# Performance work log

Hardware: AMD Instinct MI355X
Metric: run time of the kernel (lower is better)

Reference implementation:

```python
import jax, jax.numpy as jnp
import numpy as np

EPS = 1e-12  # torch F.normalize eps


def setup_inputs() -> dict:
    key = jax.random.key(0)
    k1, k2, k3, k4, k5 = jax.random.split(key, 5)
    N, C, H, W = 32, 512, 32, 32
    E = 1024   # expansion * dim
    G = 8      # group
    D = E // G # 128, per-group channel dim
    K = 64     # num_clusters
    x = jax.random.normal(k1, (N, C, H, W), dtype=jnp.float32)
    W1 = jax.random.normal(k2, (E, C), dtype=jnp.float32) / np.sqrt(C)
    W2 = jax.random.normal(k3, (G, E), dtype=jnp.float32) / np.sqrt(E)
    Wc = jax.random.normal(k4, (K, D), dtype=jnp.float32) / np.sqrt(D)
    centroids = jax.random.uniform(k5, (K, D), dtype=jnp.float32)
    return {"x": x, "W1": W1, "W2": W2, "Wc": Wc, "centroids": centroids}


def reference(x, W1, W2, Wc, centroids):
    # x: [N, C, H, W]; W1: [E, C]; W2: [G, E]; Wc: [K, D]; centroids: [K, D]
    N, C, H, W = x.shape
    E = W1.shape[0]
    G = W2.shape[0]
    K, D = Wc.shape
    P = H * W
    # descriptor-wise L2 normalization over channel dim
    norm = jnp.linalg.norm(x, axis=1, keepdims=True)
    x = x / jnp.maximum(norm, EPS)
    # linear1 on channels: [N, E, P]
    xe = jnp.einsum('ncp,ec->nep', x.reshape(N, C, P), W1)
    # grouped features: [N, G, D, P]
    xg = xe.reshape(N, G, D, P)
    # attention gate: sigmoid(linear2)  -> [N, G, P]
    att = jax.nn.sigmoid(jnp.einsum('nep,ge->ngp', xe, W2))
    # 1x1 conv = per-pixel matmul with cluster weights -> [N, G, K, P]
    soft_assign = jax.nn.softmax(jnp.einsum('ngdp,kd->ngkp', xg, Wc), axis=2)
    # combined per-(cluster,pixel) weight
    w = soft_assign * att[:, :, None, :]  # [N, G, K, P]
    # NetVLAD residual aggregation, algebraically decomposed to avoid the
    # giant [N,G,K,D,P] intermediate:
    #   vlad[n,k,d] = sum_{g,p} w * xg  -  centroids[k,d] * sum_{g,p} w
    agg = jnp.einsum('ngkp,ngdp->nkd', w, xg)  # [N, K, D]
    wsum = w.sum(axis=(1, 3))                  # [N, K]
    vlad = agg - wsum[:, :, None] * centroids[None]  # [N, K, D]
    return vlad.reshape(N, K * D)
```

## Files before the change

### kernel.cpp

```cpp
#include <hip/hip_runtime.h>


#define N_  32
#define C_  512
#define P_  1024
#define E_  1024
#define G_  8
#define D_  128
#define K_  64

typedef __attribute__((ext_vector_type(8))) short bf16x8;
typedef __attribute__((ext_vector_type(4))) float f32x4;

__device__ __forceinline__ unsigned short f2b(float f) {
    union { float f; unsigned u; } v; v.f = f;
    unsigned r = (v.u + 0x7FFFu + ((v.u >> 16) & 1u)) >> 16;
    return (unsigned short)r;
}
__device__ __forceinline__ float b2f(unsigned short h) {
    union { unsigned u; float f; } v; v.u = ((unsigned)h) << 16;
    return v.f;
}

__device__ __forceinline__ void gl_lds16(const void* g, void* l) {
    __builtin_amdgcn_global_load_lds(
        (const __attribute__((address_space(1))) void*)g,
        (__attribute__((address_space(3))) void*)l, 16, 0, 0);
}

#define SB  __builtin_amdgcn_sched_barrier(0)
#define BAR __builtin_amdgcn_s_barrier()
#define WAITV(n_) asm volatile("s_waitcnt vmcnt(" #n_ ")" ::: "memory")

__global__ __launch_bounds__(256) void k0_prep(const float* __restrict__ W1,
                                               const float* __restrict__ Wc,
                                               const float* __restrict__ W2,
                                               unsigned short* __restrict__ W1b,
                                               unsigned short* __restrict__ Vb,
                                               unsigned short* __restrict__ Wa) {
    int bid = blockIdx.x;
    int t = threadIdx.x;
    if (bid < 1024) {
        int i0 = bid * 512 + t;
        W1b[i0]       = f2b(W1[i0]);
        W1b[i0 + 256] = f2b(W1[i0 + 256]);
        int ch = bid & 1, k = (bid >> 1) & 63, g = bid >> 7;
        int c = ch * 256 + t;
        float acc = 0.f;
        #pragma unroll 8
        for (int d = 0; d < 128; ++d)
            acc += Wc[k * 128 + d] * W1[(g * 128 + d) * C_ + c];
        Vb[(g * 64 + k) * C_ + c] = f2b(acc);
    } else {
        __shared__ float red[256];
        int idx = bid - 1024;
        int g  = idx >> 4;
        int c0 = (idx & 15) * 32;
        int c  = c0 + (t & 31);
        int ec = t >> 5;
        float acc = 0.f;
        #pragma unroll 8
        for (int i = 0; i < 128; ++i) {
            int e = ec * 128 + i;
            acc += W2[g * E_ + e] * W1[e * C_ + c];
        }
        red[t] = acc;
        __syncthreads();
        if (t < 32) {
            float s = 0.f;
            #pragma unroll
            for (int j = 0; j < 8; ++j) s += red[j * 32 + t];
            Wa[g * C_ + c0 + t] = f2b(s);
        }
    }
}

__global__ __launch_bounds__(256) void k1_norm_transpose(const float* __restrict__ x,
                                                         unsigned short* __restrict__ xhat_t) {
    __shared__ short xc[128 * 256];
    __shared__ float red[256];
    __shared__ float rn[64];
    int n = blockIdx.y;
    int p0 = blockIdx.x * 64;
    int t = threadIdx.x;
    int ps = t & 63, cs = t >> 6;

    float ss = 0.f;
    for (int i = 0; i < 128; ++i) {
        float v = x[((size_t)(n * C_ + cs * 128 + i)) * P_ + p0 + ps];
        ss += v * v;
        xc[i * 256 + t] = (short)f2b(v);
    }
    red[t] = ss;
    __syncthreads();
    if (t < 64) {
        float s = red[t] + red[64 + t] + red[128 + t] + red[192 + t];
        rn[t] = 1.0f / fmaxf(sqrtf(s), 1e-12f);
    }
    __syncthreads();

    float r = rn[ps];
    size_t base = ((size_t)(n * P_ + p0 + ps)) * C_ + cs * 128;
    #pragma unroll
    for (int jj = 0; jj < 16; ++jj) {
        bf16x8 o;
        #pragma unroll
        for (int j = 0; j < 8; ++j)
            o[j] = (short)f2b(b2f((unsigned short)xc[(jj * 8 + j) * 256 + t]) * r);
        *(bf16x8*)&xhat_t[base + jj * 8] = o;
    }
}

__global__ __launch_bounds__(256) void k2_gemm_xe(const unsigned short* __restrict__ W1b,
                                                  const unsigned short* __restrict__ xhat_t,
                                                  unsigned short* __restrict__ xe) {
    __shared__ __align__(16) short As[128 * 64];
    __shared__ __align__(16) short Bs[128 * 64];
    int n = blockIdx.y;
    int e0 = (blockIdx.x >> 3) * 128;
    int p0 = (blockIdx.x & 7) * 128;
    int t = threadIdx.x;
    int w = t >> 6, l = t & 63, q = l >> 4, l15 = l & 15;
    int wr = w >> 1, wc = w & 1;

    f32x4 acc[4][4];
    #pragma unroll
    for (int mi = 0; mi < 4; ++mi)
        #pragma unroll
        for (int ni = 0; ni < 4; ++ni)
            acc[mi][ni] = (f32x4){0.f, 0.f, 0.f, 0.f};

    for (int ks = 0; ks < 8; ++ks) {
        int k0 = ks * 64;
        #pragma unroll
        for (int i = 0; i < 4; ++i) {
            int ch = i * 256 + t;
            int row = ch >> 3, c8 = ch & 7;
            gl_lds16(&W1b[(e0 + row) * C_ + k0 + ((c8 ^ (row & 7)) * 8)], &As[ch * 8]);
        }
        #pragma unroll
        for (int i = 0; i < 4; ++i) {
            int ch = i * 256 + t;
            int row = ch >> 3, c8 = ch & 7;
            gl_lds16(&xhat_t[((size_t)(n * P_ + p0 + row)) * C_ + k0 + ((c8 ^ (row & 7)) * 8)], &Bs[ch * 8]);
        }
        __syncthreads();

        #pragma unroll
        for (int kk = 0; kk < 2; ++kk) {
            bf16x8 af[4], bf[4];
            #pragma unroll
            for (int mi = 0; mi < 4; ++mi)
                af[mi] = *(const bf16x8*)&As[(wr * 64 + mi * 16 + l15) * 64 + (((kk * 4 + q) ^ (l15 & 7)) * 8)];
            #pragma unroll
            for (int ni = 0; ni < 4; ++ni)
                bf[ni] = *(const bf16x8*)&Bs[(wc * 64 + ni * 16 + l15) * 64 + (((kk * 4 + q) ^ (l15 & 7)) * 8)];
            #pragma unroll
            for (int mi = 0; mi < 4; ++mi)
                #pragma unroll
                for (int ni = 0; ni < 4; ++ni)
                    acc[mi][ni] = __builtin_amdgcn_mfma_f32_16x16x32_bf16(af[mi], bf[ni], acc[mi][ni], 0, 0, 0);
        }
        __syncthreads();
    }

    #pragma unroll
    for (int mi = 0; mi < 4; ++mi) {
        #pragma unroll
        for (int ni = 0; ni < 4; ++ni) {
            #pragma unroll
            for (int r = 0; r < 4; ++r) {
                int e = e0 + wr * 64 + mi * 16 + q * 4 + r;
                int p = p0 + wc * 64 + ni * 16 + l15;
                xe[((size_t)(n * E_ + e)) * P_ + p] = f2b(acc[mi][ni][r]);
            }
        }
    }
}

__global__ __launch_bounds__(256) void k3n_att(const unsigned short* __restrict__ Wa,
                                               const unsigned short* __restrict__ xhat_t,
                                               float* __restrict__ att_s) {
    __shared__ __align__(16) short xh[64 * 512];
    __shared__ __align__(16) short wal[8 * 520];
    int n = blockIdx.y;
    int p0 = blockIdx.x * 64;
    int t = threadIdx.x;
    int w = t >> 6, l = t & 63, q = l >> 4, l15 = l & 15;

    #pragma unroll
    for (int i = 0; i < 16; ++i) {
        int ch = i * 256 + t;
        int row = ch >> 6, s = ch & 63;
        gl_lds16(&xhat_t[((size_t)(n * P_ + p0 + row)) * C_ + ((s ^ (row & 7)) * 8)],
                 &xh[ch * 8]);
    }
    #pragma unroll
    for (int i = 0; i < 2; ++i) {
        int ch = i * 256 + t;
        int row = ch >> 6, c8 = ch & 63;
        gl_lds16(&Wa[row * C_ + c8 * 8], &wal[row * 520 + c8 * 8]);
    }
    __syncthreads();

    f32x4 acc = (f32x4){0.f, 0.f, 0.f, 0.f};
    const bf16x8 zf = {};
    #pragma unroll
    for (int kstep = 0; kstep < 16; ++kstep) {
        bf16x8 av = *(const bf16x8*)&wal[(l15 & 7) * 520 + (kstep * 4 + q) * 8];
        bf16x8 af = (l15 < 8) ? av : zf;
        int row = w * 16 + l15;
        bf16x8 bf = *(const bf16x8*)&xh[row * 512 + (((kstep * 4 + q) ^ (row & 7)) * 8)];
        acc = __builtin_amdgcn_mfma_f32_16x16x32_bf16(af, bf, acc, 0, 0, 0);
    }

    if (q < 2) {
        int p = p0 + w * 16 + l15;
        #pragma unroll
        for (int r = 0; r < 4; ++r) {
            int g = q * 4 + r;
            att_s[((size_t)(n * G_ + g)) * P_ + p] = 1.0f / (1.0f + __expf(-acc[r]));
        }
    }
}

__device__ __forceinline__ void stage_s(short* sb, const unsigned short* __restrict__ Vb,
                                        const unsigned short* __restrict__ xhat_t,
                                        int g, int n, int p0c, int k0, int t) {
    {
        int row = t >> 3, c8 = t & 7;
        gl_lds16(&Vb[(g * 64 + row) * C_ + k0 + ((c8 ^ (row & 7)) * 8)], &sb[t * 8]);
    }
    #pragma unroll
    for (int i = 0; i < 2; ++i) {
        int ch = i * 512 + t;
        int row = ch >> 3, c8 = ch & 7;
        gl_lds16(&xhat_t[((size_t)(n * P_ + p0c + row)) * C_ + k0 + ((c8 ^ (row & 7)) * 8)],
                 &sb[4096 + ch * 8]);
    }
}

__device__ __forceinline__ void stage_xg(short* xglds, const unsigned short* __restrict__ xe,
                                         int n, int g, int p0c, int t) {
    #pragma unroll
    for (int i = 0; i < 4; ++i) {
        int ch = i * 512 + t;
        int row = ch >> 4, c16 = ch & 15;
        gl_lds16(&xe[((size_t)(n * E_ + g * 128 + row)) * P_ + p0c + ((c16 ^ (row & 7)) * 8)],
                 &xglds[ch * 8]);
    }
}

__device__ __forceinline__ void mfma_s(f32x4 acc[4], const short* sb, int w, int q, int l15) {
    #pragma unroll
    for (int kk = 0; kk < 2; ++kk) {
        bf16x8 af[4], bfr;
        #pragma unroll
        for (int mi = 0; mi < 4; ++mi)
            af[mi] = *(const bf16x8*)&sb[(mi * 16 + l15) * 64 + (((kk * 4 + q) ^ (l15 & 7)) * 8)];
        bfr = *(const bf16x8*)&sb[4096 + (w * 16 + l15) * 64 + (((kk * 4 + q) ^ (l15 & 7)) * 8)];
        #pragma unroll
        for (int mi = 0; mi < 4; ++mi)
            acc[mi] = __builtin_amdgcn_mfma_f32_16x16x32_bf16(af[mi], bfr, acc[mi], 0, 0, 0);
    }
}

__global__ __launch_bounds__(512, 4) void k4_assign_agg(const unsigned short* __restrict__ Vb,
                                                        const unsigned short* __restrict__ xhat_t,
                                                        const unsigned short* __restrict__ xe,
                                                        const float* __restrict__ att_s,
                                                        float* __restrict__ agg_part,
                                                        float* __restrict__ wsum_part) {
    __shared__ __align__(16) char smem[81920];
    short* S0    = (short*)smem;
    short* S1    = (short*)(smem + 24576);
    short* xglds = (short*)(smem + 49152);
    short* wlds  = (short*)smem;
    float* wred  = (float*)smem;

    int b = blockIdx.y * 16 + blockIdx.x;
    int work = (b & 7) * 64 + (b >> 3);
    int n = work >> 4, g = work & 7, ph = (work >> 3) & 1;

    int t = threadIdx.x;
    int w = t >> 6, l = t & 63, q = l >> 4, l15 = l & 15;
    int kh = w >> 2, dq = w & 3;

    f32x4 acc_a[2][2];
    #pragma unroll
    for (int mi = 0; mi < 2; ++mi)
        #pragma unroll
        for (int ni = 0; ni < 2; ++ni)
            acc_a[mi][ni] = (f32x4){0.f, 0.f, 0.f, 0.f};
    float wsp[16];
    #pragma unroll
    for (int j = 0; j < 16; ++j) wsp[j] = 0.f;

#define RND(CUR, NXT, KN) \
    stage_s(NXT, Vb, xhat_t, g, n, p0c, (KN) * 64, t); \
    WAITV(3); BAR; SB; \
    mfma_s(acc_s, CUR, w, q, l15); \
    BAR; SB;

    #pragma unroll 1
    for (int cc = 0; cc < 4; ++cc) {
        int p0c = ph * 512 + cc * 128;

        float av = att_s[(((size_t)(n * G_ + g)) * P_) + p0c + w * 16 + l15];

        f32x4 acc_s[4];
        #pragma unroll
        for (int mi = 0; mi < 4; ++mi)
            acc_s[mi] = (f32x4){0.f, 0.f, 0.f, 0.f};

        stage_s(S0, Vb, xhat_t, g, n, p0c, 0, t);
        RND(S0, S1, 1)
        RND(S1, S0, 2)
        RND(S0, S1, 3)
        RND(S1, S0, 4)
        RND(S0, S1, 5)
        RND(S1, S0, 6)
        stage_s(S1, Vb, xhat_t, g, n, p0c, 448, t);
        stage_xg(xglds, xe, n, g, p0c, t);
        WAITV(7); BAR; SB;
        mfma_s(acc_s, S0, w, q, l15);
        BAR; SB;
        WAITV(4); BAR; SB;
        mfma_s(acc_s, S1, w, q, l15);
        BAR; SB;

        {
            float m = -1e30f;
            #pragma unroll
            for (int mi = 0; mi < 4; ++mi)
                #pragma unroll
                for (int r = 0; r < 4; ++r)
                    m = fmaxf(m, acc_s[mi][r]);
            m = fmaxf(m, __shfl_xor(m, 16));
            m = fmaxf(m, __shfl_xor(m, 32));
            float s = 0.f;
            #pragma unroll
            for (int mi = 0; mi < 4; ++mi)
                #pragma unroll
                for (int r = 0; r < 4; ++r) {
                    float e = __expf(acc_s[mi][r] - m);
                    acc_s[mi][r] = e;
                    s += e;
                }
            s += __shfl_xor(s, 16);
            s += __shfl_xor(s, 32);

            float scale = av / s;

            #pragma unroll
            for (int mi = 0; mi < 4; ++mi)
                #pragma unroll
                for (int r = 0; r < 4; ++r) {
                    float wv = acc_s[mi][r] * scale;
                    wsp[mi * 4 + r] += wv;
                    wlds[(mi * 16 + q * 4 + r) * 136 + (w * 16 + l15)] = (short)f2b(wv);
                }
        }
        __syncthreads();

        #pragma unroll
        for (int pk = 0; pk < 4; ++pk) {
            bf16x8 a2[2], b2[2];
            #pragma unroll
            for (int mi = 0; mi < 2; ++mi)
                a2[mi] = *(const bf16x8*)&wlds[(kh * 32 + mi * 16 + l15) * 136 + pk * 32 + q * 8];
            #pragma unroll
            for (int ni = 0; ni < 2; ++ni)
                b2[ni] = *(const bf16x8*)&xglds[(dq * 32 + ni * 16 + l15) * 128
                                                + (((pk * 4 + q) ^ (l15 & 7)) * 8)];
            #pragma unroll
            for (int mi = 0; mi < 2; ++mi)
                #pragma unroll
                for (int ni = 0; ni < 2; ++ni)
                    acc_a[mi][ni] = __builtin_amdgcn_mfma_f32_16x16x32_bf16(a2[mi], b2[ni], acc_a[mi][ni], 0, 0, 0);
        }
        __syncthreads();
    }

    size_t base = (((size_t)(n * G_ + g)) * 2 + ph) * 64;
    #pragma unroll
    for (int mi = 0; mi < 2; ++mi)
        #pragma unroll
        for (int ni = 0; ni < 2; ++ni)
            #pragma unroll
            for (int r = 0; r < 4; ++r) {
                int k = kh * 32 + mi * 16 + q * 4 + r;
                int d = dq * 32 + ni * 16 + l15;
                agg_part[(base + k) * 128 + d] = acc_a[mi][ni][r];
            }

    #pragma unroll
    for (int j = 0; j < 16; ++j) {
        float v = wsp[j];
        v += __shfl_xor(v, 1);
        v += __shfl_xor(v, 2);
        v += __shfl_xor(v, 4);
        v += __shfl_xor(v, 8);
        if (l15 == 0) {
            int k = (j >> 2) * 16 + q * 4 + (j & 3);
            wred[w * 64 + k] = v;
        }
    }
    __syncthreads();
    if (t < 64) {
        float s = 0.f;
        #pragma unroll
        for (int wv = 0; wv < 8; ++wv)
            s += wred[wv * 64 + t];
        wsum_part[(((size_t)(n * G_ + g)) * 2 + ph) * 64 + t] = s;
    }
}

__global__ __launch_bounds__(256) void k5_final(const float* __restrict__ agg_part,
                                                const float* __restrict__ wsum_part,
                                                const float* __restrict__ centroids,
                                                float* __restrict__ out) {
    int idx = blockIdx.x * 256 + threadIdx.x;
    int d = idx & 127;
    int k = (idx >> 7) & 63;
    int n = idx >> 13;
    float ws = 0.f;
    #pragma unroll
    for (int g = 0; g < 8; ++g)
        #pragma unroll
        for (int ph = 0; ph < 2; ++ph)
            ws += wsum_part[(((size_t)(n * G_ + g)) * 2 + ph) * 64 + k];
    float agg = 0.f;
    #pragma unroll
    for (int g = 0; g < 8; ++g)
        #pragma unroll
        for (int ph = 0; ph < 2; ++ph)
            agg += agg_part[(((((size_t)(n * G_ + g)) * 2 + ph) * 64) + k) * 128 + d];
    out[idx] = agg - ws * centroids[k * 128 + d];
}

extern "C" void kernel_launch(void* const* d_in, const int* in_sizes, int n_in,
                              void* d_out, int out_size, void* d_ws, size_t ws_size,
                              hipStream_t stream) {
    const float* x         = (const float*)d_in[0];
    const float* W1        = (const float*)d_in[1];
    const float* W2        = (const float*)d_in[2];
    const float* Wc        = (const float*)d_in[3];
    const float* centroids = (const float*)d_in[4];
    float* out = (float*)d_out;

    char* ws = (char*)d_ws;
    unsigned short* W1b      = (unsigned short*)(ws + 0);
    unsigned short* Vb       = (unsigned short*)(ws + 1048576);
    unsigned short* xhat_t   = (unsigned short*)(ws + 1572864);
    unsigned short* xe       = (unsigned short*)(ws + 35127296);
    float*          att_s    = (float*)(ws + 102236160);
    float*          agg_part = (float*)(ws + 103284736);
    float*          wsum_part= (float*)(ws + 120061952);
    unsigned short* Wa       = (unsigned short*)(ws + 120193024);

    hipLaunchKernelGGL(k0_prep,        dim3(1152), dim3(256), 0, stream, W1, Wc, W2, W1b, Vb, Wa);
    hipLaunchKernelGGL(k1_norm_transpose, dim3(16, 32), dim3(256), 0, stream, x, xhat_t);
    hipLaunchKernelGGL(k2_gemm_xe,     dim3(64, 32), dim3(256), 0, stream, W1b, xhat_t, xe);
    hipLaunchKernelGGL(k3n_att,        dim3(16, 32), dim3(256), 0, stream, Wa, xhat_t, att_s);
    hipLaunchKernelGGL(k4_assign_agg,  dim3(16, 32), dim3(512), 0, stream, Vb, xhat_t, xe,
                       att_s, agg_part, wsum_part);
    hipLaunchKernelGGL(k5_final,       dim3(1024), dim3(256), 0, stream,
                       agg_part, wsum_part, centroids, out);
}
```

Measured before the change: 214.5 us.

## Fuse xe GEMM into assign-aggregate kernel, computing xg tiles on the fly

Removes the standalone k2 GEMM that wrote the bf16 xe tensor (64MB) to global memory. The assign/aggregate kernel now stages W1b slices alongside Vb and xhat, computes the per-group xg tile with extra MFMAs inside the same K loop, and writes it into LDS for the aggregation GEMM. This cuts the xe write and re-read traffic and one kernel launch. In exchange the fused kernel does more MFMA work and uses more LDS per stage and more registers, which may lower occupancy.

```diff
diff --git a/kernel.cpp b/kernel.cpp
--- a/kernel.cpp
+++ b/kernel.cpp
@@ -111,73 +111,6 @@
     }
 }
 
-__global__ __launch_bounds__(256) void k2_gemm_xe(const unsigned short* __restrict__ W1b,
-                                                  const unsigned short* __restrict__ xhat_t,
-                                                  unsigned short* __restrict__ xe) {
-    __shared__ __align__(16) short As[128 * 64];
-    __shared__ __align__(16) short Bs[128 * 64];
-    int n = blockIdx.y;
-    int e0 = (blockIdx.x >> 3) * 128;
-    int p0 = (blockIdx.x & 7) * 128;
-    int t = threadIdx.x;
-    int w = t >> 6, l = t & 63, q = l >> 4, l15 = l & 15;
-    int wr = w >> 1, wc = w & 1;
-
-    f32x4 acc[4][4];
-    #pragma unroll
-    for (int mi = 0; mi < 4; ++mi)
-        #pragma unroll
-        for (int ni = 0; ni < 4; ++ni)
-            acc[mi][ni] = (f32x4){0.f, 0.f, 0.f, 0.f};
-
-    for (int ks = 0; ks < 8; ++ks) {
-        int k0 = ks * 64;
-        #pragma unroll
-        for (int i = 0; i < 4; ++i) {
-            int ch = i * 256 + t;
-            int row = ch >> 3, c8 = ch & 7;
-            gl_lds16(&W1b[(e0 + row) * C_ + k0 + ((c8 ^ (row & 7)) * 8)], &As[ch * 8]);
-        }
-        #pragma unroll
-        for (int i = 0; i < 4; ++i) {
-            int ch = i * 256 + t;
-            int row = ch >> 3, c8 = ch & 7;
-            gl_lds16(&xhat_t[((size_t)(n * P_ + p0 + row)) * C_ + k0 + ((c8 ^ (row & 7)) * 8)], &Bs[ch * 8]);
-        }
-        __syncthreads();
-
-        #pragma unroll
-        for (int kk = 0; kk < 2; ++kk) {
-            bf16x8 af[4], bf[4];
-            #pragma unroll
-            for (int mi = 0; mi < 4; ++mi)
-                af[mi] = *(const bf16x8*)&As[(wr * 64 + mi * 16 + l15) * 64 + (((kk * 4 + q) ^ (l15 & 7)) * 8)];
-            #pragma unroll
-            for (int ni = 0; ni < 4; ++ni)
-                bf[ni] = *(const bf16x8*)&Bs[(wc * 64 + ni * 16 + l15) * 64 + (((kk * 4 + q) ^ (l15 & 7)) * 8)];
-            #pragma unroll
-            for (int mi = 0; mi < 4; ++mi)
-                #pragma unroll
-                for (int ni = 0; ni < 4; ++ni)
-                    acc[mi][ni] = __builtin_amdgcn_mfma_f32_16x16x32_bf16(af[mi], bf[ni], acc[mi][ni], 0, 0, 0);
-        }
-        __syncthreads();
-    }
-
-    #pragma unroll
-    for (int mi = 0; mi < 4; ++mi) {
-        #pragma unroll
-        for (int ni = 0; ni < 4; ++ni) {
-            #pragma unroll
-            for (int r = 0; r < 4; ++r) {
-                int e = e0 + wr * 64 + mi * 16 + q * 4 + r;
-                int p = p0 + wc * 64 + ni * 16 + l15;
-                xe[((size_t)(n * E_ + e)) * P_ + p] = f2b(acc[mi][ni][r]);
-            }
-        }
-    }
-}
-
 __global__ __launch_bounds__(256) void k3n_att(const unsigned short* __restrict__ Wa,
                                                const unsigned short* __restrict__ xhat_t,
                                                float* __restrict__ att_s) {
@@ -224,9 +157,11 @@
     }
 }
 
-__device__ __forceinline__ void stage_s(short* sb, const unsigned short* __restrict__ Vb,
-                                        const unsigned short* __restrict__ xhat_t,
-                                        int g, int n, int p0c, int k0, int t) {
+__device__ __forceinline__ void stage_s3(short* sb,
+                                         const unsigned short* __restrict__ Vb,
+                                         const unsigned short* __restrict__ W1b,
+                                         const unsigned short* __restrict__ xhat_t,
+                                         int g, int n, int p0c, int k0, int t) {
     {
         int row = t >> 3, c8 = t & 7;
         gl_lds16(&Vb[(g * 64 + row) * C_ + k0 + ((c8 ^ (row & 7)) * 8)], &sb[t * 8]);
@@ -238,45 +173,54 @@
         gl_lds16(&xhat_t[((size_t)(n * P_ + p0c + row)) * C_ + k0 + ((c8 ^ (row & 7)) * 8)],
                  &sb[4096 + ch * 8]);
     }
-}
-
-__device__ __forceinline__ void stage_xg(short* xglds, const unsigned short* __restrict__ xe,
-                                         int n, int g, int p0c, int t) {
-    #pragma unroll
-    for (int i = 0; i < 4; ++i) {
+    #pragma unroll
+    for (int i = 0; i < 2; ++i) {
         int ch = i * 512 + t;
-        int row = ch >> 4, c16 = ch & 15;
-        gl_lds16(&xe[((size_t)(n * E_ + g * 128 + row)) * P_ + p0c + ((c16 ^ (row & 7)) * 8)],
-                 &xglds[ch * 8]);
-    }
-}
-
-__device__ __forceinline__ void mfma_s(f32x4 acc[4], const short* sb, int w, int q, int l15) {
+        int row = ch >> 3, c8 = ch & 7;
+        gl_lds16(&W1b[(g * 128 + row) * C_ + k0 + ((c8 ^ (row & 7)) * 8)],
+                 &sb[12288 + ch * 8]);
+    }
+}
+
+__device__ __forceinline__ void mfma_sx(f32x4 accs[4], f32x4 accx[4][2], const short* sb,
+                                        int w, int wd, int wp, int q, int l15) {
     #pragma unroll
     for (int kk = 0; kk < 2; ++kk) {
-        bf16x8 af[4], bfr;
+        int col = ((kk * 4 + q) ^ (l15 & 7)) * 8;
+        bf16x8 af[4], bfr, axf[4], bxf[2];
         #pragma unroll
         for (int mi = 0; mi < 4; ++mi)
-            af[mi] = *(const bf16x8*)&sb[(mi * 16 + l15) * 64 + (((kk * 4 + q) ^ (l15 & 7)) * 8)];
-        bfr = *(const bf16x8*)&sb[4096 + (w * 16 + l15) * 64 + (((kk * 4 + q) ^ (l15 & 7)) * 8)];
+            af[mi] = *(const bf16x8*)&sb[(mi * 16 + l15) * 64 + col];
+        bfr = *(const bf16x8*)&sb[4096 + (w * 16 + l15) * 64 + col];
         #pragma unroll
         for (int mi = 0; mi < 4; ++mi)
-            acc[mi] = __builtin_amdgcn_mfma_f32_16x16x32_bf16(af[mi], bfr, acc[mi], 0, 0, 0);
-    }
-}
-
-__global__ __launch_bounds__(512, 4) void k4_assign_agg(const unsigned short* __restrict__ Vb,
-                                                        const unsigned short* __restrict__ xhat_t,
-                                                        const unsigned short* __restrict__ xe,
-                                                        const float* __restrict__ att_s,
-                                                        float* __restrict__ agg_part,
-                                                        float* __restrict__ wsum_part) {
+            axf[mi] = *(const bf16x8*)&sb[12288 + (wd * 64 + mi * 16 + l15) * 64 + col];
+        #pragma unroll
+        for (int ni = 0; ni < 2; ++ni)
+            bxf[ni] = *(const bf16x8*)&sb[4096 + (wp * 32 + ni * 16 + l15) * 64 + col];
+        #pragma unroll
+        for (int mi = 0; mi < 4; ++mi)
+            accs[mi] = __builtin_amdgcn_mfma_f32_16x16x32_bf16(af[mi], bfr, accs[mi], 0, 0, 0);
+        #pragma unroll
+        for (int mi = 0; mi < 4; ++mi)
+            #pragma unroll
+            for (int ni = 0; ni < 2; ++ni)
+                accx[mi][ni] = __builtin_amdgcn_mfma_f32_16x16x32_bf16(axf[mi], bxf[ni], accx[mi][ni], 0, 0, 0);
+    }
+}
+
+__global__ __launch_bounds__(512, 4) void k4_fused(const unsigned short* __restrict__ Vb,
+                                                   const unsigned short* __restrict__ W1b,
+                                                   const unsigned short* __restrict__ xhat_t,
+                                                   const float* __restrict__ att_s,
+                                                   float* __restrict__ agg_part,
+                                                   float* __restrict__ wsum_part) {
     __shared__ __align__(16) char smem[81920];
-    short* S0    = (short*)smem;
-    short* S1    = (short*)(smem + 24576);
-    short* xglds = (short*)(smem + 49152);
-    short* wlds  = (short*)smem;
-    float* wred  = (float*)smem;
+    short* S0   = (short*)smem;
+    short* S1   = (short*)(smem + 40960);
+    short* wlds = (short*)smem;
+    short* xgb  = (short*)(smem + 40960);
+    float* wred = (float*)smem;
 
     int b = blockIdx.y * 16 + blockIdx.x;
     int work = (b & 7) * 64 + (b >> 3);
@@ -285,6 +229,7 @@
     int t = threadIdx.x;
     int w = t >> 6, l = t & 63, q = l >> 4, l15 = l & 15;
     int kh = w >> 2, dq = w & 3;
+    int wd = w >> 2, wp = w & 3;
 
     f32x4 acc_a[2][2];
     #pragma unroll
@@ -297,9 +242,9 @@
     for (int j = 0; j < 16; ++j) wsp[j] = 0.f;
 
 #define RND(CUR, NXT, KN) \
-    stage_s(NXT, Vb, xhat_t, g, n, p0c, (KN) * 64, t); \
-    WAITV(3); BAR; SB; \
-    mfma_s(acc_s, CUR, w, q, l15); \
+    stage_s3(NXT, Vb, W1b, xhat_t, g, n, p0c, (KN) * 64, t); \
+    WAITV(5); BAR; SB; \
+    mfma_sx(acc_s, acc_x, CUR, w, wd, wp, q, l15); \
     BAR; SB;
 
     #pragma unroll 1
@@ -309,24 +254,25 @@
         float av = att_s[(((size_t)(n * G_ + g)) * P_) + p0c + w * 16 + l15];
 
         f32x4 acc_s[4];
-        #pragma unroll
-        for (int mi = 0; mi < 4; ++mi)
+        f32x4 acc_x[4][2];
+        #pragma unroll
+        for (int mi = 0; mi < 4; ++mi) {
             acc_s[mi] = (f32x4){0.f, 0.f, 0.f, 0.f};
-
-        stage_s(S0, Vb, xhat_t, g, n, p0c, 0, t);
+            #pragma unroll
+            for (int ni = 0; ni < 2; ++ni)
+                acc_x[mi][ni] = (f32x4){0.f, 0.f, 0.f, 0.f};
+        }
+
+        stage_s3(S0, Vb, W1b, xhat_t, g, n, p0c, 0, t);
         RND(S0, S1, 1)
         RND(S1, S0, 2)
         RND(S0, S1, 3)
         RND(S1, S0, 4)
         RND(S0, S1, 5)
         RND(S1, S0, 6)
-        stage_s(S1, Vb, xhat_t, g, n, p0c, 448, t);
-        stage_xg(xglds, xe, n, g, p0c, t);
-        WAITV(7); BAR; SB;
-        mfma_s(acc_s, S0, w, q, l15);
-        BAR; SB;
-        WAITV(4); BAR; SB;
-        mfma_s(acc_s, S1, w, q, l15);
+        RND(S0, S1, 7)
+        WAITV(0); BAR; SB;
+        mfma_sx(acc_s, acc_x, S1, w, wd, wp, q, l15);
         BAR; SB;
 
         {
@@ -361,6 +307,17 @@
                     wlds[(mi * 16 + q * 4 + r) * 136 + (w * 16 + l15)] = (short)f2b(wv);
                 }
         }
+
+        #pragma unroll
+        for (int mi = 0; mi < 4; ++mi)
+            #pragma unroll
+            for (int ni = 0; ni < 2; ++ni)
+                #pragma unroll
+                for (int r = 0; r < 4; ++r) {
+                    int d = wd * 64 + mi * 16 + q * 4 + r;
+                    int p = wp * 32 + ni * 16 + l15;
+                    xgb[d * 128 + (((p >> 3) ^ (d & 7)) * 8) + (p & 7)] = (short)f2b(acc_x[mi][ni][r]);
+                }
         __syncthreads();
 
         #pragma unroll
@@ -371,8 +328,8 @@
                 a2[mi] = *(const bf16x8*)&wlds[(kh * 32 + mi * 16 + l15) * 136 + pk * 32 + q * 8];
             #pragma unroll
             for (int ni = 0; ni < 2; ++ni)
-                b2[ni] = *(const bf16x8*)&xglds[(dq * 32 + ni * 16 + l15) * 128
-                                                + (((pk * 4 + q) ^ (l15 & 7)) * 8)];
+                b2[ni] = *(const bf16x8*)&xgb[(dq * 32 + ni * 16 + l15) * 128
+                                              + (((pk * 4 + q) ^ (l15 & 7)) * 8)];
             #pragma unroll
             for (int mi = 0; mi < 2; ++mi)
                 #pragma unroll
@@ -453,7 +410,6 @@
     unsigned short* W1b      = (unsigned short*)(ws + 0);
     unsigned short* Vb       = (unsigned short*)(ws + 1048576);
     unsigned short* xhat_t   = (unsigned short*)(ws + 1572864);
-    unsigned short* xe       = (unsigned short*)(ws + 35127296);
     float*          att_s    = (float*)(ws + 102236160);
     float*          agg_part = (float*)(ws + 103284736);
     float*          wsum_part= (float*)(ws + 120061952);
@@ -461,9 +417,8 @@
 
     hipLaunchKernelGGL(k0_prep,        dim3(1152), dim3(256), 0, stream, W1, Wc, W2, W1b, Vb, Wa);
     hipLaunchKernelGGL(k1_norm_transpose, dim3(16, 32), dim3(256), 0, stream, x, xhat_t);
-    hipLaunchKernelGGL(k2_gemm_xe,     dim3(64, 32), dim3(256), 0, stream, W1b, xhat_t, xe);
     hipLaunchKernelGGL(k3n_att,        dim3(16, 32), dim3(256), 0, stream, Wa, xhat_t, att_s);
-    hipLaunchKernelGGL(k4_assign_agg,  dim3(16, 32), dim3(512), 0, stream, Vb, xhat_t, xe,
+    hipLaunchKernelGGL(k4_fused,       dim3(16, 32), dim3(512), 0, stream, Vb, W1b, xhat_t,
                        att_s, agg_part, wsum_part);
     hipLaunchKernelGGL(k5_final,       dim3(1024), dim3(256), 0, stream,
                        agg_part, wsum_part, centroids, out);
```

Result: slower. 284.6 us (+32.7%).
